# Kernel tuning notes

Hardware: AMD Instinct MI355X
Metric: run time of the kernel (lower is better)

Reference implementation:

```python
import jax, jax.numpy as jnp
import numpy as np

# mamba-370m-style dims (n_layers reduced for tractable reference execution)
H = 1024      # hidden_size
DI = 2048     # intermediate (expand*H)
DS = 16       # ssm state size
DTR = 64      # time_step_rank = H/16
NL = 4        # layers
V = 50280     # vocab after resize_token_embeddings
LLM = 4096    # llm_input_size
B, L = 4, 1024
MEM_ID = 50279
STRIDE = 64
K = L // STRIDE  # mem tokens per sequence
EPS = 1e-5


def setup_inputs() -> dict:
    key = jax.random.key(0)
    ks = jax.random.split(key, 10)
    s = 0.02
    ids = jax.random.randint(ks[0], (B, L), 0, MEM_ID)
    ids = ids.at[:, STRIDE - 1::STRIDE].set(MEM_ID)  # K mem tokens per row
    return {
        "input_ids": ids,
        "embed": jax.random.normal(ks[1], (V, H)) * s,
        "norm_w": jnp.ones((NL, H)),
        "in_proj_w": jax.random.normal(ks[2], (NL, 2 * DI, H)) * s,
        "conv_w": jax.random.normal(ks[3], (NL, DI, 4)) * s,
        "conv_b": jnp.zeros((NL, DI)),
        "x_proj_w": jax.random.normal(ks[4], (NL, DTR + 2 * DS, DI)) * s,
        "dt_w": jax.random.normal(ks[5], (NL, DI, DTR)) * s,
        "dt_b": jax.random.uniform(ks[6], (NL, DI), minval=-4.0, maxval=-2.0),
        "A_log": jnp.log(jnp.broadcast_to(jnp.arange(1, DS + 1, dtype=jnp.float32), (NL, DI, DS))),
        "D": jnp.ones((NL, DI)),
        "out_proj_w": jax.random.normal(ks[7], (NL, H, DI)) * s,
        "final_norm_w": jnp.ones((H,)),
        "proj_w": jax.random.normal(ks[8], (LLM, H)) * s,
        "proj_b": jnp.zeros((LLM,)),
    }


def rmsnorm(x, w):
    return x * jax.lax.rsqrt(jnp.mean(x * x, axis=-1, keepdims=True) + EPS) * w


def mamba_layer(h, p):
    norm_w, in_w, cw, cb, xw, dtw, dtb, A_log, Dp, ow = p
    x = rmsnorm(h, norm_w)
    xz = jnp.einsum('blh,dh->bld', x, in_w)          # (B,L,2*DI)
    x, z = jnp.split(xz, 2, axis=-1)
    # causal depthwise conv1d, kernel 4, left pad 3
    xt = jnp.transpose(x, (0, 2, 1))                  # (B,DI,L)
    xc = jax.lax.conv_general_dilated(xt, cw[:, None, :], (1,), [(3, 0)],
                                      feature_group_count=DI)
    u = jax.nn.silu(xc + cb[None, :, None])
    u = jnp.transpose(u, (0, 2, 1))                   # (B,L,DI)
    ssm = jnp.einsum('bld,ed->ble', u, xw)            # (B,L,DTR+2*DS)
    dt_raw = ssm[..., :DTR]
    Bm = ssm[..., DTR:DTR + DS]
    Cm = ssm[..., DTR + DS:]
    dt = jax.nn.softplus(jnp.einsum('blr,dr->bld', dt_raw, dtw) + dtb)  # (B,L,DI)
    A = -jnp.exp(A_log)                               # (DI,DS)

    def step(s, inp):
        dt_t, B_t, C_t, u_t = inp                     # (B,DI),(B,DS),(B,DS),(B,DI)
        dA = jnp.exp(dt_t[..., None] * A)             # (B,DI,DS)
        s = s * dA + (dt_t * u_t)[..., None] * B_t[:, None, :]
        return s, jnp.einsum('bds,bs->bd', s, C_t)

    s0 = jnp.zeros((h.shape[0], DI, DS), dtype=h.dtype)
    _, ys = jax.lax.scan(step, s0, (dt.swapaxes(0, 1), Bm.swapaxes(0, 1),
                                    Cm.swapaxes(0, 1), u.swapaxes(0, 1)))
    y = ys.swapaxes(0, 1) + u * Dp
    y = y * jax.nn.silu(z)
    return h + jnp.einsum('bld,hd->blh', y, ow), None


def reference(input_ids, embed, norm_w, in_proj_w, conv_w, conv_b, x_proj_w,
              dt_w, dt_b, A_log, D, out_proj_w, final_norm_w, proj_w, proj_b):
    h = embed[input_ids]                              # (B,L,H)
    h, _ = jax.lax.scan(mamba_layer, h,
                        (norm_w, in_proj_w, conv_w, conv_b, x_proj_w,
                         dt_w, dt_b, A_log, D, out_proj_w))
    h = rmsnorm(h, final_norm_w)
    # gather mem-token positions (K per row, in order); stable argsort puts mask hits first
    mask = input_ids == MEM_ID
    pos = jnp.argsort(jnp.where(mask, 0, 1), axis=1)[:, :K]
    feats = jnp.take_along_axis(h, pos[:, :, None], axis=1)   # (B,K,H)
    return jnp.einsum('bkh,lh->bkl', feats, proj_w) + proj_b  # (B,K,LLM)
```

## Files before the change

kernel.cpp:

```cpp
#include <hip/hip_runtime.h>
#include <hip/hip_bf16.h>
#include <cstdint>
#include <cstddef>

#define H_    1024
#define DI_   2048
#define DS_   16
#define DTR_  64
#define NL_   4
#define LLM_  4096
#define B_    4
#define L_    1024
#define MEMID 50279
#define KTOK  16
#define MROWS (B_*L_)
#define BK    64

using bf16 = __hip_bfloat16;
typedef __attribute__((ext_vector_type(8))) short short8;
typedef __attribute__((ext_vector_type(4))) short short4v;
typedef __attribute__((ext_vector_type(4))) float floatx4;
typedef __attribute__((ext_vector_type(4))) unsigned int uint4v;

__device__ __forceinline__ float b2f(bf16 v){ return __bfloat162float(v); }
__device__ __forceinline__ bf16  f2b(float v){ return __float2bfloat16(v); }
__device__ __forceinline__ float sh2f(short s){
    unsigned u = ((unsigned)(unsigned short)s) << 16;
    return __builtin_bit_cast(float, u);
}
__device__ __forceinline__ short f2sh(float v){
    bf16 b = f2b(v);
    return __builtin_bit_cast(short, b);
}
__device__ __forceinline__ float bcf(unsigned int u){ return __builtin_bit_cast(float, u); }

__device__ __forceinline__ float rowsum16(float v){
    float t;
    asm("v_add_f32_dpp %0, %1, %1 row_shr:1 row_mask:0xf bank_mask:0xf bound_ctrl:0" : "=v"(t) : "v"(v));
    asm("v_add_f32_dpp %0, %1, %1 row_shr:2 row_mask:0xf bank_mask:0xf bound_ctrl:0" : "=v"(v) : "v"(t));
    asm("v_add_f32_dpp %0, %1, %1 row_shr:4 row_mask:0xf bank_mask:0xf bound_ctrl:0" : "=v"(t) : "v"(v));
    asm("v_add_f32_dpp %0, %1, %1 row_shr:8 row_mask:0xf bank_mask:0xf bound_ctrl:0" : "=v"(v) : "v"(t));
    return v;
}

__device__ __forceinline__ void async16(bf16* l, const bf16* g){
    __builtin_amdgcn_global_load_lds(
        (const __attribute__((address_space(1))) void*)g,
        (__attribute__((address_space(3))) void*)l,
        16, 0, 0);
}

__global__ void cvt_kernel(const float* __restrict__ src, bf16* __restrict__ dst, int n4)
{
    int i = blockIdx.x*256 + threadIdx.x;
    if (i < n4){
        float4 f = ((const float4*)src)[i];
        short4v o; o[0]=f2sh(f.x); o[1]=f2sh(f.y); o[2]=f2sh(f.z); o[3]=f2sh(f.w);
        ((short4v*)dst)[i] = o;
    }
}

__global__ void cvt4_kernel(const float* __restrict__ s0, bf16* __restrict__ d0, int t0,
                            const float* __restrict__ s1, bf16* __restrict__ d1, int t1,
                            const float* __restrict__ s2, bf16* __restrict__ d2, int t2,
                            const float* __restrict__ s3, bf16* __restrict__ d3, int t3)
{
    int i = blockIdx.x*256 + threadIdx.x;
    const float* s; bf16* d; int local;
    if      (i < t0){ s=s0; d=d0; local=i; }
    else if (i < t1){ s=s1; d=d1; local=i-t0; }
    else if (i < t2){ s=s2; d=d2; local=i-t1; }
    else if (i < t3){ s=s3; d=d3; local=i-t2; }
    else return;
    float4 f = ((const float4*)s)[local];
    short4v o; o[0]=f2sh(f.x); o[1]=f2sh(f.y); o[2]=f2sh(f.z); o[3]=f2sh(f.w);
    ((short4v*)d)[local] = o;
}

__global__ void embed_kernel(const int* __restrict__ ids,
                             const float* __restrict__ emb,
                             float* __restrict__ h)
{
    int row = blockIdx.x;
    int id  = ids[row];
    const float4* src = (const float4*)(emb + (size_t)id * H_);
    float4* dst = (float4*)(h + (size_t)row * H_);
    dst[threadIdx.x] = src[threadIdx.x];
}

__global__ void rmsnorm_kernel(const float* __restrict__ h,
                               const float* __restrict__ w,
                               bf16* __restrict__ out)
{
    int row = blockIdx.x;
    const float* x = h + (size_t)row * H_;
    float v[4]; float ss = 0.f;
    #pragma unroll
    for (int i = 0; i < 4; i++){ v[i] = x[threadIdx.x + 256*i]; ss += v[i]*v[i]; }
    #pragma unroll
    for (int off = 32; off; off >>= 1) ss += __shfl_down(ss, off, 64);
    __shared__ float red[4];
    __shared__ float scale_s;
    int lane = threadIdx.x & 63, wv = threadIdx.x >> 6;
    if (lane == 0) red[wv] = ss;
    __syncthreads();
    if (threadIdx.x == 0){
        float t = red[0]+red[1]+red[2]+red[3];
        scale_s = rsqrtf(t * (1.f/H_) + 1e-5f);
    }
    __syncthreads();
    float sc = scale_s;
    #pragma unroll
    for (int i = 0; i < 4; i++){
        int c = threadIdx.x + 256*i;
        out[(size_t)row*H_ + c] = f2b(v[i] * sc * w[c]);
    }
}

__launch_bounds__(256)
__global__ void gemm_bt(const bf16* __restrict__ A, int lda,
                        const bf16* __restrict__ Bm, int ldb,
                        int M, int N, int K,
                        float* __restrict__ Cf, bf16* __restrict__ Cb, int ldc,
                        const float* __restrict__ bias, int mode)
{
    __shared__ __align__(16) bf16 sA[128*BK];
    __shared__ __align__(16) bf16 sB[128*BK];

    int tid  = threadIdx.x;
    int lane = tid & 63;
    int wv   = tid >> 6;
    int quad = lane >> 4, r16 = lane & 15;
    int m0 = blockIdx.y*128, n0 = blockIdx.x*128;
    int wm = (wv>>1)*64, wn = (wv&1)*64;

    int rr = tid >> 3;
    int kc = ((tid & 7) ^ (rr & 7)) * 8;
    const bf16* pA = A  + (size_t)(m0 + rr)*lda + kc;
    const bf16* pB = Bm + (size_t)(n0 + rr)*ldb + kc;
    bf16* lA = sA + wv*512;
    bf16* lB = sB + wv*512;

    floatx4 acc[4][4];
    #pragma unroll
    for (int i=0;i<4;i++)
        #pragma unroll
        for (int j=0;j<4;j++) acc[i][j] = (floatx4){0.f,0.f,0.f,0.f};

    for (int k0 = 0; k0 < K; k0 += BK){
        async16(lA,        pA);
        async16(lA + 2048, pA + (size_t)32*lda);
        async16(lA + 4096, pA + (size_t)64*lda);
        async16(lA + 6144, pA + (size_t)96*lda);
        async16(lB,        pB);
        async16(lB + 2048, pB + (size_t)32*ldb);
        async16(lB + 4096, pB + (size_t)64*ldb);
        async16(lB + 6144, pB + (size_t)96*ldb);
        pA += BK; pB += BK;
        __syncthreads();

        #pragma unroll
        for (int kk=0; kk<2; kk++){
            short8 a[4], b[4];
            #pragma unroll
            for (int i=0;i<4;i++)
                a[i] = *(const short8*)(sA + (wm + i*16 + r16)*BK
                                          + (((kk*4+quad) ^ (r16 & 7))*8));
            #pragma unroll
            for (int j=0;j<4;j++)
                b[j] = *(const short8*)(sB + (wn + j*16 + r16)*BK
                                          + (((kk*4+quad) ^ (r16 & 7))*8));
            #pragma unroll
            for (int i=0;i<4;i++)
                #pragma unroll
                for (int j=0;j<4;j++)
                    acc[i][j] = __builtin_amdgcn_mfma_f32_16x16x32_bf16(a[i], b[j], acc[i][j], 0, 0, 0);
        }
        __syncthreads();
    }

    #pragma unroll
    for (int i=0;i<4;i++)
        #pragma unroll
        for (int j=0;j<4;j++){
            int mq = m0 + wm + i*16 + quad*4;
            int n  = n0 + wn + j*16 + r16;
            if (mode == 1){
                if (n < N){
                    short4v pk;
                    #pragma unroll
                    for (int rr2=0;rr2<4;rr2++){
                        float xx = acc[i][j][rr2] + bias[n];
                        float sp = (xx > 20.f) ? xx : log1pf(__expf(xx));
                        pk[rr2] = f2sh(sp);
                    }
                    *(short4v*)(Cb + (size_t)n*ldc + mq) = pk;
                }
            } else {
                #pragma unroll
                for (int rr2=0;rr2<4;rr2++){
                    int m = mq + rr2;
                    if (m < M && n < N){
                        float v = acc[i][j][rr2];
                        if (mode == 0)      Cf[(size_t)m*ldc + n] = v + (bias ? bias[n] : 0.f);
                        else if (mode == 2) Cf[(size_t)m*ldc + n] += v;
                        else                Cb[(size_t)m*ldc + n] = f2b(v);
                    }
                }
            }
        }
}

__launch_bounds__(256)
__global__ void gemm_ssm(const bf16* __restrict__ A,
                         const bf16* __restrict__ Bm,
                         bf16* __restrict__ dtA,
                         bf16* __restrict__ pBt,
                         bf16* __restrict__ pCt)
{
    __shared__ __align__(16) bf16 sA2[32*64];
    __shared__ __align__(16) bf16 sB2[96*64];

    int tid  = threadIdx.x;
    int lane = tid & 63;
    int wv   = tid >> 6;
    int quad = lane >> 4, r16 = lane & 15;
    int m0 = blockIdx.x * 32;
    int wr = wv >> 1, wc = wv & 1;

    int ar = tid >> 3;
    int kc = ((tid & 7) ^ (ar & 7)) * 8;
    const bf16* pA  = A  + (size_t)(m0 + ar)*DI_ + kc;
    const bf16* pB0 = Bm + (size_t)(ar)     *DI_ + kc;
    const bf16* pB1 = Bm + (size_t)(32 + ar)*DI_ + kc;
    const bf16* pB2 = Bm + (size_t)(64 + ar)*DI_ + kc;
    bf16* lA  = sA2 + wv*512;
    bf16* lB0 = sB2 + wv*512;
    bf16* lB1 = sB2 + 2048 + wv*512;
    bf16* lB2 = sB2 + 4096 + wv*512;

    floatx4 acc[3];
    #pragma unroll
    for (int j=0;j<3;j++) acc[j] = (floatx4){0.f,0.f,0.f,0.f};

    for (int k0 = 0; k0 < DI_; k0 += 64){
        async16(lA,  pA);
        async16(lB0, pB0);
        async16(lB1, pB1);
        async16(lB2, pB2);
        pA += 64; pB0 += 64; pB1 += 64; pB2 += 64;
        __syncthreads();
        #pragma unroll
        for (int kk=0; kk<2; kk++){
            short8 a = *(const short8*)(sA2 + (wr*16 + r16)*64
                                            + (((kk*4+quad) ^ (r16 & 7))*8));
            #pragma unroll
            for (int j=0;j<3;j++){
                short8 b = *(const short8*)(sB2 + (wc*48 + j*16 + r16)*64
                                                + (((kk*4+quad) ^ (r16 & 7))*8));
                acc[j] = __builtin_amdgcn_mfma_f32_16x16x32_bf16(a, b, acc[j], 0, 0, 0);
            }
        }
        __syncthreads();
    }

    int mq = m0 + wr*16 + quad*4;
    #pragma unroll
    for (int j=0;j<3;j++){
        int n = wc*48 + j*16 + r16;
        if (n < 64){
            #pragma unroll
            for (int rr=0;rr<4;rr++)
                dtA[(size_t)(mq+rr)*64 + n] = f2b(acc[j][rr]);
        } else if (n < 80){
            short4v pk;
            #pragma unroll
            for (int rr=0;rr<4;rr++) pk[rr] = f2sh(acc[j][rr]);
            *(short4v*)(pBt + (size_t)(n-64)*MROWS + mq) = pk;
        } else {
            short4v pk;
            #pragma unroll
            for (int rr=0;rr<4;rr++) pk[rr] = f2sh(acc[j][rr]);
            *(short4v*)(pCt + (size_t)(n-80)*MROWS + mq) = pk;
        }
    }
}

__global__ void conv_silu_kernel(const bf16* __restrict__ xz,
                                 const float* __restrict__ cw,
                                 const float* __restrict__ cb,
                                 bf16* __restrict__ u,
                                 bf16* __restrict__ u_t)
{
    __shared__ float tile[64][65];
    int bt0 = blockIdx.x * 64;
    int d0  = blockIdx.y * 64;
    int tid = threadIdx.x;
    const short8 z8 = {0,0,0,0,0,0,0,0};
    #pragma unroll
    for (int it = 0; it < 2; it++){
        int task = it*256 + tid;
        int g    = task & 7;
        int tr   = task >> 3;
        int row  = bt0 + tr;
        int t    = row & (L_-1);
        int d8   = d0 + g*8;
        const bf16* base = xz + (size_t)row*(2*DI_) + d8;
        short8 x3 = *(const short8*)(base);
        short8 x2 = (t>=1) ? *(const short8*)(base - 1*(2*DI_)) : z8;
        short8 x1 = (t>=2) ? *(const short8*)(base - 2*(2*DI_)) : z8;
        short8 x0 = (t>=3) ? *(const short8*)(base - 3*(2*DI_)) : z8;
        short8 out;
        #pragma unroll
        for (int j=0;j<8;j++){
            int d = d8 + j;
            float4 w4 = ((const float4*)cw)[d];
            float acc = cb[d];
            acc += sh2f(x0[j])*w4.x;
            acc += sh2f(x1[j])*w4.y;
            acc += sh2f(x2[j])*w4.z;
            acc += sh2f(x3[j])*w4.w;
            float s = acc / (1.f + __expf(-acc));
            out[j] = f2sh(s);
            tile[g*8+j][tr] = s;
        }
        *(short8*)(u + (size_t)row*DI_ + d8) = out;
    }
    __syncthreads();
    #pragma unroll
    for (int it = 0; it < 2; it++){
        int task = it*256 + tid;
        int g    = task & 7;
        int dr   = task >> 3;
        int tc8  = g*8;
        short8 o;
        #pragma unroll
        for (int j=0;j<8;j++) o[j] = f2sh(tile[dr][tc8+j]);
        *(short8*)(u_t + (size_t)(d0+dr)*MROWS + bt0 + tc8) = o;
    }
}

#define SCAN_GROUP(dtv,uv,bv,cv,gidx) { \
    uint4v yo; \
    _Pragma("unroll") \
    for (int j = 0; j < 4; j++){ \
        unsigned int wdt = (dtv)[j], wu = (uv)[j], wB = (bv)[j], wC = (cv)[j]; \
        float dt0 = bcf(wdt << 16), u0 = bcf(wu << 16); \
        float b0  = bcf(wB  << 16), c0 = bcf(wC << 16); \
        float e0; asm("v_exp_f32 %0, %1" : "=v"(e0) : "v"(dt0 * A2)); \
        state = __builtin_fmaf(state, e0, dt0 * u0 * b0); \
        float y0 = __builtin_fmaf(u0, Dv, rowsum16(state * c0)); \
        float dt1 = bcf(wdt & 0xffff0000u), u1 = bcf(wu & 0xffff0000u); \
        float b1  = bcf(wB  & 0xffff0000u), c1 = bcf(wC & 0xffff0000u); \
        float e1; asm("v_exp_f32 %0, %1" : "=v"(e1) : "v"(dt1 * A2)); \
        state = __builtin_fmaf(state, e1, dt1 * u1 * b1); \
        float y1 = __builtin_fmaf(u1, Dv, rowsum16(state * c1)); \
        unsigned int pk; \
        asm("v_cvt_pk_bf16_f32 %0, %1, %2" : "=v"(pk) : "v"(y0), "v"(y1)); \
        yo[j] = pk; \
    } \
    if (s_idx == 15) yp_[gidx] = yo; \
}

__global__ void scan_kernel(const bf16* __restrict__ dt_t,
                            const bf16* __restrict__ u_t,
                            const bf16* __restrict__ sB_t,
                            const bf16* __restrict__ sC_t,
                            const float* __restrict__ A_log,
                            const float* __restrict__ Dp,
                            bf16* __restrict__ y_t)
{
    int lane  = threadIdx.x & 63;
    int wv    = threadIdx.x >> 6;
    int s_idx = lane & 15;
    int ch    = lane >> 4;
    int c = blockIdx.x*16 + wv*4 + ch;
    int d = c & (DI_-1);
    int b = c >> 11;
    float A2 = -__expf(A_log[d*DS_ + s_idx]) * 1.4426950408889634f;
    float Dv = Dp[d];
    const uint4v* dtp = (const uint4v*)(dt_t + (size_t)d*MROWS + b*L_);
    const uint4v* utp = (const uint4v*)(u_t  + (size_t)d*MROWS + b*L_);
    const uint4v* Bp  = (const uint4v*)(sB_t + (size_t)s_idx*MROWS + b*L_);
    const uint4v* Cp  = (const uint4v*)(sC_t + (size_t)s_idx*MROWS + b*L_);
    uint4v* yp_ = (uint4v*)(y_t + (size_t)d*MROWS + b*L_);

    const int NG = L_/8;
    float state = 0.f;

    uint4v dA = dtp[0], uA = utp[0], bA = Bp[0], cA = Cp[0];
    uint4v dB = dtp[1], uB = utp[1], bB = Bp[1], cB = Cp[1];
    uint4v dC = dtp[2], uC = utp[2], bC = Bp[2], cC = Cp[2];
    uint4v dD = dtp[3], uD = utp[3], bD = Bp[3], cD = Cp[3];

    for (int g = 0; g < NG; g += 4){
        int p0 = g+4 < NG ? g+4 : NG-1;
        int p1 = g+5 < NG ? g+5 : NG-1;
        int p2 = g+6 < NG ? g+6 : NG-1;
        int p3 = g+7 < NG ? g+7 : NG-1;
        SCAN_GROUP(dA, uA, bA, cA, g);
        dA = dtp[p0]; uA = utp[p0]; bA = Bp[p0]; cA = Cp[p0];
        SCAN_GROUP(dB, uB, bB, cB, g+1);
        dB = dtp[p1]; uB = utp[p1]; bB = Bp[p1]; cB = Cp[p1];
        SCAN_GROUP(dC, uC, bC, cC, g+2);
        dC = dtp[p2]; uC = utp[p2]; bC = Bp[p2]; cC = Cp[p2];
        SCAN_GROUP(dD, uD, bD, cD, g+3);
        dD = dtp[p3]; uD = utp[p3]; bD = Bp[p3]; cD = Cp[p3];
    }
}

__global__ void gate_kernel(const bf16* __restrict__ y_t,
                            bf16* __restrict__ xz)
{
    __shared__ float tile[64][65];
    int bt0 = blockIdx.x * 64;
    int d0  = blockIdx.y * 64;
    int tid = threadIdx.x;
    #pragma unroll
    for (int it = 0; it < 16; it++){
        int idx = it*256 + tid;
        int tc  = idx & 63;
        int dr  = idx >> 6;
        tile[dr][tc] = b2f(y_t[(size_t)(d0+dr)*MROWS + bt0 + tc]);
    }
    __syncthreads();
    #pragma unroll
    for (int it = 0; it < 16; it++){
        int idx = it*256 + tid;
        int dd  = idx & 63;
        int tr  = idx >> 6;
        int row = bt0 + tr;
        float z  = b2f(xz[(size_t)row*(2*DI_) + DI_ + d0 + dd]);
        float sz = z / (1.f + __expf(-z));
        xz[(size_t)row*(2*DI_) + d0 + dd] = f2b(tile[dd][tr] * sz);
    }
}

__global__ void pos_kernel(const int* __restrict__ ids, int* __restrict__ pos)
{
    int b = blockIdx.x;
    __shared__ int cnt[256];
    int t = threadIdx.x;
    int local = 0;
    #pragma unroll
    for (int i=0;i<4;i++)
        if (ids[b*L_ + t*4 + i] == MEMID) local++;
    cnt[t] = local;
    __syncthreads();
    if (t == 0){
        int run = 0;
        for (int i=0;i<256;i++){ int tmp = cnt[i]; cnt[i] = run; run += tmp; }
    }
    __syncthreads();
    int rank = cnt[t];
    #pragma unroll
    for (int i=0;i<4;i++){
        int l = t*4 + i;
        if (ids[b*L_ + l] == MEMID){
            if (rank < KTOK) pos[b*KTOK + rank] = l;
            rank++;
        }
    }
}

__global__ void featnorm_kernel(const float* __restrict__ h,
                                const float* __restrict__ w,
                                const int* __restrict__ pos,
                                bf16* __restrict__ feats)
{
    int bk = blockIdx.x;
    int row = (bk >> 4) * L_ + pos[bk];
    const float* x = h + (size_t)row * H_;
    float v[4]; float ss = 0.f;
    #pragma unroll
    for (int i = 0; i < 4; i++){ v[i] = x[threadIdx.x + 256*i]; ss += v[i]*v[i]; }
    #pragma unroll
    for (int off = 32; off; off >>= 1) ss += __shfl_down(ss, off, 64);
    __shared__ float red[4];
    __shared__ float scale_s;
    int lane = threadIdx.x & 63, wv = threadIdx.x >> 6;
    if (lane == 0) red[wv] = ss;
    __syncthreads();
    if (threadIdx.x == 0){
        float t = red[0]+red[1]+red[2]+red[3];
        scale_s = rsqrtf(t * (1.f/H_) + 1e-5f);
    }
    __syncthreads();
    float sc = scale_s;
    #pragma unroll
    for (int i = 0; i < 4; i++){
        int c = threadIdx.x + 256*i;
        feats[(size_t)bk*H_ + c] = f2b(v[i] * sc * w[c]);
    }
}

extern "C" void kernel_launch(void* const* d_in, const int* in_sizes, int n_in,
                              void* d_out, int out_size, void* d_ws, size_t ws_size,
                              hipStream_t stream)
{
    const int*   ids    = (const int*)  d_in[0];
    const float* emb    = (const float*)d_in[1];
    const float* norm_w = (const float*)d_in[2];
    const float* in_w   = (const float*)d_in[3];
    const float* cw     = (const float*)d_in[4];
    const float* cb     = (const float*)d_in[5];
    const float* xw     = (const float*)d_in[6];
    const float* dtw    = (const float*)d_in[7];
    const float* dtb    = (const float*)d_in[8];
    const float* A_log  = (const float*)d_in[9];
    const float* Dp     = (const float*)d_in[10];
    const float* ow     = (const float*)d_in[11];
    const float* fnw    = (const float*)d_in[12];
    const float* projw  = (const float*)d_in[13];
    const float* projb  = (const float*)d_in[14];
    float* out          = (float*)d_out;

    char* ws = (char*)d_ws;
    float* h     = (float*)(ws + 0);
    bf16*  xn    = (bf16*) (ws + 16777216);
    bf16*  wb_in = (bf16*) (ws + 25165824);
    bf16*  u     = (bf16*) (ws + 16777216);
    bf16*  dt_t  = (bf16*) (ws + 16777216);
    bf16*  xz    = (bf16*) (ws + 33554432);
    bf16*  u_t   = (bf16*) (ws + 67108864);
    bf16*  y_t   = (bf16*) (ws + 83886080);
    bf16*  dtA   = (bf16*) (ws + 100663296);
    bf16*  sB_t  = (bf16*) (ws + 101187584);
    bf16*  sC_t  = (bf16*) (ws + 101318656);
    bf16*  fe    = (bf16*) (ws + 101449728);
    int*   pos   = (int*)  (ws + 101580800);
    bf16*  wb_ow = (bf16*) (ws + 101581056);
    bf16*  wb_xw = (bf16*) (ws + 105775360);
    bf16*  wb_dtw= (bf16*) (ws + 106168576);

    embed_kernel<<<MROWS, 256, 0, stream>>>(ids, emb, h);

    const int n_in_w  = 2*DI_*H_;
    const int n_ow_w  = H_*DI_;
    const int n_xw_w  = 96*DI_;
    const int n_dtw_w = DI_*DTR_;
    const int t0c = n_in_w>>2;
    const int t1c = t0c + (n_ow_w>>2);
    const int t2c = t1c + (n_xw_w>>2);
    const int t3c = t2c + (n_dtw_w>>2);

    for (int l = 0; l < NL_; l++){
        const float* nw_l  = norm_w + l*H_;
        const float* cw_l  = cw     + l*DI_*4;
        const float* cb_l  = cb     + l*DI_;
        const float* dtb_l = dtb    + l*DI_;
        const float* al_l  = A_log  + l*DI_*DS_;
        const float* Dp_l  = Dp     + l*DI_;

        cvt4_kernel<<<(t3c+255)/256, 256, 0, stream>>>(
            in_w + (size_t)l*n_in_w, wb_in, t0c,
            ow   + (size_t)l*n_ow_w, wb_ow, t1c,
            xw   + (size_t)l*n_xw_w, wb_xw, t2c,
            dtw  + (size_t)l*n_dtw_w, wb_dtw, t3c);

        rmsnorm_kernel<<<MROWS, 256, 0, stream>>>(h, nw_l, xn);
        gemm_bt<<<dim3(32,32), 256, 0, stream>>>(xn, H_, wb_in, H_,
                                                 MROWS, 2*DI_, H_,
                                                 nullptr, xz, 2*DI_, nullptr, 3);
        conv_silu_kernel<<<dim3(MROWS/64, DI_/64), 256, 0, stream>>>(xz, cw_l, cb_l, u, u_t);
        gemm_ssm<<<128, 256, 0, stream>>>(u, wb_xw, dtA, sB_t, sC_t);
        gemm_bt<<<dim3(16,32), 256, 0, stream>>>(dtA, DTR_, wb_dtw, DTR_,
                                                 MROWS, DI_, DTR_,
                                                 nullptr, dt_t, MROWS, dtb_l, 1);
        scan_kernel<<<512, 256, 0, stream>>>(dt_t, u_t, sB_t, sC_t, al_l, Dp_l, y_t);
        gate_kernel<<<dim3(MROWS/64, DI_/64), 256, 0, stream>>>(y_t, xz);
        gemm_bt<<<dim3(8,32), 256, 0, stream>>>(xz, 2*DI_, wb_ow, DI_,
                                                MROWS, H_, DI_,
                                                h, nullptr, H_, nullptr, 2);
    }

    pos_kernel<<<B_, 256, 0, stream>>>(ids, pos);
    featnorm_kernel<<<B_*KTOK, 256, 0, stream>>>(h, fnw, pos, fe);
    cvt_kernel<<<((LLM_*H_/4)+255)/256, 256, 0, stream>>>(projw, wb_in, LLM_*H_/4);
    gemm_bt<<<dim3(32,1), 256, 0, stream>>>(fe, H_, wb_in, H_,
                                            B_*KTOK, LLM_, H_,
                                            out, nullptr, LLM_, projb, 0);
}
```

Baseline: 1.581 ms.

## Add narrower out-proj GEMM for more blocks and vectorize rmsnorm and gate

Replaces the out-projection gemm_bt launch (8x32 blocks of 128x128 tiles) with a specialized gemm_out using 128x64 tiles, doubling the grid to 512 blocks so more compute units stay busy on the 4096x1024x2048 GEMM. It also vectorizes rmsnorm loads and stores with float4 and short4, and makes the gate kernel read and write 8 bf16 values per access. The smaller N tile lowers reuse of each A tile and doubles A reads. The new kernel hardcodes its dimensions and has no bounds checks.

Result: faster. 1.454 ms (-8.1%).

```diff
diff --git a/kernel.cpp b/kernel.cpp
--- a/kernel.cpp
+++ b/kernel.cpp
@@ -93,10 +93,8 @@
                                bf16* __restrict__ out)
 {
     int row = blockIdx.x;
-    const float* x = h + (size_t)row * H_;
-    float v[4]; float ss = 0.f;
-    #pragma unroll
-    for (int i = 0; i < 4; i++){ v[i] = x[threadIdx.x + 256*i]; ss += v[i]*v[i]; }
+    float4 v = ((const float4*)(h + (size_t)row * H_))[threadIdx.x];
+    float ss = v.x*v.x + v.y*v.y + v.z*v.z + v.w*v.w;
     #pragma unroll
     for (int off = 32; off; off >>= 1) ss += __shfl_down(ss, off, 64);
     __shared__ float red[4];
@@ -110,11 +108,13 @@
     }
     __syncthreads();
     float sc = scale_s;
-    #pragma unroll
-    for (int i = 0; i < 4; i++){
-        int c = threadIdx.x + 256*i;
-        out[(size_t)row*H_ + c] = f2b(v[i] * sc * w[c]);
-    }
+    float4 w4 = ((const float4*)w)[threadIdx.x];
+    short4v o;
+    o[0] = f2sh(v.x * sc * w4.x);
+    o[1] = f2sh(v.y * sc * w4.y);
+    o[2] = f2sh(v.z * sc * w4.z);
+    o[3] = f2sh(v.w * sc * w4.w);
+    ((short4v*)(out + (size_t)row*H_))[threadIdx.x] = o;
 }
 
 __launch_bounds__(256)
@@ -212,6 +212,76 @@
 }
 
 __launch_bounds__(256)
+__global__ void gemm_out(const bf16* __restrict__ A, int lda,
+                         const bf16* __restrict__ Bm, int ldb,
+                         float* __restrict__ Cf, int ldc)
+{
+    __shared__ __align__(16) bf16 sA[128*BK];
+    __shared__ __align__(16) bf16 sB[64*BK];
+
+    int tid  = threadIdx.x;
+    int lane = tid & 63;
+    int wv   = tid >> 6;
+    int quad = lane >> 4, r16 = lane & 15;
+    int m0 = blockIdx.y*128, n0 = blockIdx.x*64;
+    int wm = (wv>>1)*64, wn = (wv&1)*32;
+
+    int rr = tid >> 3;
+    int kc = ((tid & 7) ^ (rr & 7)) * 8;
+    const bf16* pA = A  + (size_t)(m0 + rr)*lda + kc;
+    const bf16* pB = Bm + (size_t)(n0 + rr)*ldb + kc;
+    bf16* lA = sA + wv*512;
+    bf16* lB = sB + wv*512;
+
+    floatx4 acc[4][2];
+    #pragma unroll
+    for (int i=0;i<4;i++)
+        #pragma unroll
+        for (int j=0;j<2;j++) acc[i][j] = (floatx4){0.f,0.f,0.f,0.f};
+
+    for (int k0 = 0; k0 < DI_; k0 += BK){
+        async16(lA,        pA);
+        async16(lA + 2048, pA + (size_t)32*lda);
+        async16(lA + 4096, pA + (size_t)64*lda);
+        async16(lA + 6144, pA + (size_t)96*lda);
+        async16(lB,        pB);
+        async16(lB + 2048, pB + (size_t)32*ldb);
+        pA += BK; pB += BK;
+        __syncthreads();
+
+        #pragma unroll
+        for (int kk=0; kk<2; kk++){
+            short8 a[4], b[2];
+            #pragma unroll
+            for (int i=0;i<4;i++)
+                a[i] = *(const short8*)(sA + (wm + i*16 + r16)*BK
+                                          + (((kk*4+quad) ^ (r16 & 7))*8));
+            #pragma unroll
+            for (int j=0;j<2;j++)
+                b[j] = *(const short8*)(sB + (wn + j*16 + r16)*BK
+                                          + (((kk*4+quad) ^ (r16 & 7))*8));
+            #pragma unroll
+            for (int i=0;i<4;i++)
+                #pragma unroll
+                for (int j=0;j<2;j++)
+                    acc[i][j] = __builtin_amdgcn_mfma_f32_16x16x32_bf16(a[i], b[j], acc[i][j], 0, 0, 0);
+        }
+        __syncthreads();
+    }
+
+    #pragma unroll
+    for (int i=0;i<4;i++)
+        #pragma unroll
+        for (int j=0;j<2;j++){
+            int mq = m0 + wm + i*16 + quad*4;
+            int n  = n0 + wn + j*16 + r16;
+            #pragma unroll
+            for (int rr2=0;rr2<4;rr2++)
+                Cf[(size_t)(mq+rr2)*ldc + n] += acc[i][j][rr2];
+        }
+}
+
+__launch_bounds__(256)
 __global__ void gemm_ssm(const bf16* __restrict__ A,
                          const bf16* __restrict__ Bm,
                          bf16* __restrict__ dtA,
@@ -417,22 +487,31 @@
     int d0  = blockIdx.y * 64;
     int tid = threadIdx.x;
     #pragma unroll
-    for (int it = 0; it < 16; it++){
-        int idx = it*256 + tid;
-        int tc  = idx & 63;
-        int dr  = idx >> 6;
-        tile[dr][tc] = b2f(y_t[(size_t)(d0+dr)*MROWS + bt0 + tc]);
-    }
-    __syncthreads();
-    #pragma unroll
-    for (int it = 0; it < 16; it++){
-        int idx = it*256 + tid;
-        int dd  = idx & 63;
-        int tr  = idx >> 6;
-        int row = bt0 + tr;
-        float z  = b2f(xz[(size_t)row*(2*DI_) + DI_ + d0 + dd]);
-        float sz = z / (1.f + __expf(-z));
-        xz[(size_t)row*(2*DI_) + d0 + dd] = f2b(tile[dd][tr] * sz);
+    for (int it = 0; it < 2; it++){
+        int task = it*256 + tid;
+        int g    = task & 7;
+        int dr   = task >> 3;
+        short8 v = *(const short8*)(y_t + (size_t)(d0+dr)*MROWS + bt0 + g*8);
+        #pragma unroll
+        for (int j=0;j<8;j++) tile[dr][g*8+j] = sh2f(v[j]);
+    }
+    __syncthreads();
+    #pragma unroll
+    for (int it = 0; it < 2; it++){
+        int task = it*256 + tid;
+        int g    = task & 7;
+        int tr   = task >> 3;
+        int row  = bt0 + tr;
+        int d8   = g*8;
+        short8 z8 = *(const short8*)(xz + (size_t)row*(2*DI_) + DI_ + d0 + d8);
+        short8 o;
+        #pragma unroll
+        for (int j=0;j<8;j++){
+            float z  = sh2f(z8[j]);
+            float sz = z / (1.f + __expf(-z));
+            o[j] = f2sh(tile[d8+j][tr] * sz);
+        }
+        *(short8*)(xz + (size_t)row*(2*DI_) + d0 + d8) = o;
     }
 }
 
@@ -569,9 +648,7 @@
                                                  nullptr, dt_t, MROWS, dtb_l, 1);
         scan_kernel<<<512, 256, 0, stream>>>(dt_t, u_t, sB_t, sC_t, al_l, Dp_l, y_t);
         gate_kernel<<<dim3(MROWS/64, DI_/64), 256, 0, stream>>>(y_t, xz);
-        gemm_bt<<<dim3(8,32), 256, 0, stream>>>(xz, 2*DI_, wb_ow, DI_,
-                                                MROWS, H_, DI_,
-                                                h, nullptr, H_, nullptr, 2);
+        gemm_out<<<dim3(16,32), 256, 0, stream>>>(xz, 2*DI_, wb_ow, DI_, h, H_);
     }
 
     pos_kernel<<<B_, 256, 0, stream>>>(ids, pos);
```
